# Kernel tuning notes

Measured on AMD Instinct MI355X. Metric: run time of the kernel, lower is better.

## Reference

```python
import jax, jax.numpy as jnp
import numpy as np

N_QUBITS = 8
INPUT_DIM = 256
SEQ_LEN = 256
BATCH = 512


def qgate(theta, x):
    # Closed-form expectation of the PennyLane circuit:
    #   RX(x_i) then RY(theta_i) on each wire (from |0>), then CNOT chain 0->1->...->n-1,
    #   measure <Z_k>.  Single-wire <Z_j> = cos(x_j) * cos(theta_j); CNOT chain maps
    #   Z_k -> Z_0 Z_1 ... Z_k in the Heisenberg picture, so on the product state
    #   <Z_k> = prod_{j<=k} cos(x_j) cos(theta_j).
    # x: (B, n_wires), theta: (n_wires,)
    return jnp.cumprod(jnp.cos(x) * jnp.cos(theta), axis=-1)


def setup_inputs() -> dict:
    key = jax.random.key(0)
    ks = jax.random.split(key, 14)
    d_in = INPUT_DIM + N_QUBITS  # concat([x, hx]) -> 264
    lin_scale = 1.0 / np.sqrt(d_in)
    inp = {
        "inputs": jax.random.normal(ks[0], (SEQ_LEN, BATCH, INPUT_DIM), dtype=jnp.float32),
        "Wf": jax.random.normal(ks[1], (N_QUBITS, d_in), dtype=jnp.float32) * lin_scale,
        "bf": jax.random.normal(ks[2], (N_QUBITS,), dtype=jnp.float32) * lin_scale,
        "Wi": jax.random.normal(ks[3], (N_QUBITS, d_in), dtype=jnp.float32) * lin_scale,
        "bi": jax.random.normal(ks[4], (N_QUBITS,), dtype=jnp.float32) * lin_scale,
        "Wu": jax.random.normal(ks[5], (N_QUBITS, d_in), dtype=jnp.float32) * lin_scale,
        "bu": jax.random.normal(ks[6], (N_QUBITS,), dtype=jnp.float32) * lin_scale,
        "Wo": jax.random.normal(ks[7], (N_QUBITS, d_in), dtype=jnp.float32) * lin_scale,
        "bo": jax.random.normal(ks[8], (N_QUBITS,), dtype=jnp.float32) * lin_scale,
        "pf": jax.random.normal(ks[9], (N_QUBITS,), dtype=jnp.float32),
        "pi_": jax.random.normal(ks[10], (N_QUBITS,), dtype=jnp.float32),
        "pu": jax.random.normal(ks[11], (N_QUBITS,), dtype=jnp.float32),
        "po": jax.random.normal(ks[12], (N_QUBITS,), dtype=jnp.float32),
    }
    return inp


def reference(inputs, Wf, bf, Wi, bi, Wu, bu, Wo, bo, pf, pi_, pu, po):
    B = inputs.shape[1]
    H = pf.shape[0]  # hidden_dim == n_qubits

    def step(carry, x):
        hx, cx = carry
        comb = jnp.concatenate([x, hx], axis=1)  # (B, input_dim + H)
        f = jax.nn.sigmoid(qgate(pf, comb @ Wf.T + bf))
        i = jax.nn.sigmoid(qgate(pi_, comb @ Wi.T + bi))
        g = jnp.tanh(qgate(pu, comb @ Wu.T + bu))
        o = jax.nn.sigmoid(qgate(po, comb @ Wo.T + bo))
        cx = f * cx + i * g
        hx = o * jnp.tanh(cx)
        return (hx, cx), hx

    init = (jnp.zeros((B, H), dtype=inputs.dtype), jnp.zeros((B, H), dtype=inputs.dtype))
    (hx, cx), stacked = jax.lax.scan(step, init, inputs)
    return stacked, hx, cx
```

## Files before the change

kernel.cpp:

```cpp
#include <hip/hip_runtime.h>
#include <hip/hip_bf16.h>


#define SEQ   256
#define BATCH 512
#define DIN   256
#define NROWS (SEQ * BATCH)
#define DCOMB 264
#define ZSTR  34

typedef __attribute__((ext_vector_type(8))) short short8;
typedef __attribute__((ext_vector_type(4))) float f32x4;
typedef __attribute__((ext_vector_type(2))) float f32x2;

__device__ __forceinline__ short f2bf(float f) {
    union { __hip_bfloat16 h; short s; } u;
    u.h = __float2bfloat16(f);
    return u.s;
}
__device__ __forceinline__ float bf2f(short s) {
    union { short s; __hip_bfloat16 h; } u;
    u.s = s;
    return __bfloat162float(u.h);
}

__device__ __forceinline__ short8 pack8(float4 a, float4 b) {
    union { short8 s8; int i[4]; } u;
    union { __hip_bfloat162 h; int i; } v;
    v.h = __float22bfloat162_rn(make_float2(a.x, a.y)); u.i[0] = v.i;
    v.h = __float22bfloat162_rn(make_float2(a.z, a.w)); u.i[1] = v.i;
    v.h = __float22bfloat162_rn(make_float2(b.x, b.y)); u.i[2] = v.i;
    v.h = __float22bfloat162_rn(make_float2(b.z, b.w)); u.i[3] = v.i;
    return u.s8;
}

#define DPP_ROR(V, S) \
    __int_as_float(__builtin_amdgcn_update_dpp(__float_as_int(V), __float_as_int(V), 0x120 | (S), 0xF, 0xF, false))
#define QP(V, CTRL) \
    __int_as_float(__builtin_amdgcn_update_dpp(__float_as_int(V), __float_as_int(V), (CTRL), 0xF, 0xF, false))
#define PSTG2(A, D) { \
    float s0_ = __int_as_float(__builtin_amdgcn_update_dpp(one_i, __float_as_int(A.x), 0x110 | (D), 0xF, 0xF, false)); \
    float s1_ = __int_as_float(__builtin_amdgcn_update_dpp(one_i, __float_as_int(A.y), 0x110 | (D), 0xF, 0xF, false)); \
    A *= (f32x2){s0_, s1_}; }

__global__ __launch_bounds__(512, 2) void qlstm_fused(
    const float* __restrict__ X,
    const float* __restrict__ Wf, const float* __restrict__ Wi,
    const float* __restrict__ Wu, const float* __restrict__ Wo,
    const float* __restrict__ bfv, const float* __restrict__ biv,
    const float* __restrict__ buv, const float* __restrict__ bov,
    const float* __restrict__ pf, const float* __restrict__ pi_,
    const float* __restrict__ pu, const float* __restrict__ po,
    float* __restrict__ out)
{
    __shared__ short8 Wl[2048];
    __shared__ float Zl[516 * ZSTR];
    __shared__ float Hl[SEQ * 16];

    const int tx  = threadIdx.x;
    const int l   = tx & 63;
    const int wid = tx >> 6;
    const int lm  = l & 15;
    const int lk  = l >> 4;
    const int B0  = blockIdx.x;

    const float* Wg[4] = {Wf, Wi, Wu, Wo};
    const float* Bg[4] = {bfv, biv, buv, bov};

    #pragma unroll
    for (int e = 0; e < 4; ++e) {
        const int ent  = tx + e * 512;
        const int lane = ent & 63;
        const int ks   = (ent >> 6) & 7;
        const int hl   = (ent >> 9) & 1;
        const int nt   = (ent >> 10) & 1;
        const int elm  = lane & 15, elk = lane >> 4;
        const int c    = nt * 16 + elm;
        const float* wrow = Wg[c & 3] + (c >> 2) * DCOMB + ks * 32 + elk * 8;
        short8 fr;
        #pragma unroll
        for (int j = 0; j < 8; ++j) {
            const float v = wrow[j];
            const short h16 = f2bf(v);
            fr[j] = hl ? f2bf(v - bf2f(h16)) : h16;
        }
        Wl[ent] = fr;
    }

    float bias0, bias1;
    { const int c0 = lm;      bias0 = Bg[c0 & 3][c0 >> 2];
      const int c1 = 16 + lm; bias1 = Bg[c1 & 3][c1 >> 2]; }

    __syncthreads();

    #pragma unroll
    for (int p = 0; p < 4; ++p) {
        const int r0 = p * 128 + wid * 16;
        const int r  = r0 + lm;
        const float* xbase =
            X + ((long)(r >> 1) * BATCH + B0 * 2 + (r & 1)) * DIN + lk * 8;

        float4 xv[16];
        #pragma unroll
        for (int i = 0; i < 16; ++i)
            xv[i] = *(const float4*)(xbase + (i >> 1) * 32 + (i & 1) * 4);

        f32x4 acc0 = (f32x4){bias0, bias0, bias0, bias0};
        f32x4 acc1 = (f32x4){bias1, bias1, bias1, bias1};
        #pragma unroll
        for (int ks = 0; ks < 8; ++ks) {
            const short8 a = pack8(xv[2 * ks], xv[2 * ks + 1]);
            acc0 = __builtin_amdgcn_mfma_f32_16x16x32_bf16(a, Wl[ks * 64 + l],        acc0, 0, 0, 0);
            acc0 = __builtin_amdgcn_mfma_f32_16x16x32_bf16(a, Wl[(8  + ks) * 64 + l], acc0, 0, 0, 0);
            acc1 = __builtin_amdgcn_mfma_f32_16x16x32_bf16(a, Wl[(16 + ks) * 64 + l], acc1, 0, 0, 0);
            acc1 = __builtin_amdgcn_mfma_f32_16x16x32_bf16(a, Wl[(24 + ks) * 64 + l], acc1, 0, 0, 0);
        }

        #pragma unroll
        for (int rr = 0; rr < 4; ++rr) {
            Zl[(r0 + lk * 4 + rr) * ZSTR + lm]      = acc0[rr];
            Zl[(r0 + lk * 4 + rr) * ZSTR + 16 + lm] = acc1[rr];
        }
    }
    __syncthreads();

    if (tx < 64) {
        const int q   = tx & 15;
        const int kq  = q >> 1;
        const int hi  = q & 1;
        const int bl  = (tx >> 4) & 1;
        const int b   = B0 * 2 + bl;
        const int oidx = b * 8 + kq;
        const int woff = kq * DCOMB + DIN;

        const float* WgA = hi ? Wu : Wf;
        const float* WgB = hi ? Wo : Wi;
        f32x2 wp[8];
        #pragma unroll
        for (int s = 0; s < 8; ++s) {
            const int j = (kq - s) & 7;
            wp[s] = (f32x2){WgA[woff + j], WgB[woff + j]};
        }
        const f32x2 cth = (f32x2){__cosf((hi ? pu : pf)[kq]),
                                  __cosf((hi ? po : pi_)[kq])};

        const float SK1 = 0.25f, SK2 = -0.0208333333f, SK3 = 0.0020833333f,
                    SK4 = -0.00021082f;
        const f32x2 k0 = (f32x2){hi ? 0.0f : 0.5f, 0.5f};
        const f32x2 k1 = (f32x2){hi ? 0.9999016f : SK1, SK1};
        const f32x2 k2 = (f32x2){hi ? -0.3310485f : SK2, SK2};
        const f32x2 k3 = (f32x2){hi ? 0.1204423f : SK3, SK3};
        const f32x2 k4 = (f32x2){hi ? -0.0277012f : SK4, SK4};

        const int one_i = __float_as_int(1.0f);

        float hx = 0.0f, cx = 0.0f;
        const int zbase = bl * ZSTR + 2 * q;
        float* __restrict__ hlp = Hl + bl * 8 + kq;

        f32x2 ring0 = *(const f32x2*)&Zl[zbase];
        f32x2 ring1 = *(const f32x2*)&Zl[2 * ZSTR + zbase];

        #pragma unroll 8
        for (int t = 0; t < SEQ; ++t) {
            const f32x2 z2 = ring0;
            ring0 = ring1;
            ring1 = *(const f32x2*)&Zl[(t + 2) * (2 * ZSTR) + zbase];

            const float h0 = hx;
            const float h1 = DPP_ROR(hx, 2),  h2 = DPP_ROR(hx, 4);
            const float h3 = DPP_ROR(hx, 6),  h4 = DPP_ROR(hx, 8);
            const float h5 = DPP_ROR(hx, 10), h6 = DPP_ROR(hx, 12);
            const float h7 = DPP_ROR(hx, 14);

            f32x2 e0 = (f32x2){h0, h0} * wp[0] + (f32x2){h1, h1} * wp[1];
            f32x2 e1 = (f32x2){h2, h2} * wp[2] + (f32x2){h3, h3} * wp[3];
            f32x2 e2 = (f32x2){h4, h4} * wp[4] + (f32x2){h5, h5} * wp[5];
            f32x2 e3 = (f32x2){h6, h6} * wp[6] + (f32x2){h7, h7} * wp[7];
            const f32x2 p = ((z2 + e0) + (e1 + e2)) + e3;

            f32x2 A = (f32x2){__cosf(p.x), __cosf(p.y)} * cth;
            PSTG2(A, 2) PSTG2(A, 4) PSTG2(A, 8)

            const f32x2 t2 = A * A;
            f32x2 rr = k3 + t2 * k4;
            rr = k2 + t2 * rr;
            rr = k1 + t2 * rr;
            const f32x2 P = k0 + A * rr;

            const float f_all = QP(P.x, 0xA0);
            const float u_all = QP(P.x, 0xF5);
            const float i_all = QP(P.y, 0xA0);
            const float o_all = QP(P.y, 0xF5);

            cx = fmaf(f_all, cx, i_all * u_all);

            const float tq  = cx * cx;
            const float num = cx * fmaf(tq, fmaf(tq, 1.0f, 105.0f), 945.0f);
            const float den = fmaf(tq, fmaf(tq, 15.0f, 420.0f), 945.0f);
            const float tc  = num * __builtin_amdgcn_rcpf(den);

            hx = o_all * tc;

            hlp[t * 16] = hx;
        }
        if (hi == 0 && tx < 32) {
            out[NROWS * 8 + oidx]        = hx;
            out[NROWS * 8 + 4096 + oidx] = cx;
        }
    }
    __syncthreads();

    {
        const int f0 = tx * 8;
        const int t  = f0 >> 4;
        const int c  = f0 & 15;
        const float4* src = (const float4*)&Hl[f0];
        float4* dst = (float4*)(out + (long)t * (BATCH * 8) + B0 * 16 + c);
        dst[0] = src[0];
        dst[1] = src[1];
    }
}

extern "C" void kernel_launch(void* const* d_in, const int* in_sizes, int n_in,
                              void* d_out, int out_size, void* d_ws, size_t ws_size,
                              hipStream_t stream) {
    const float* X   = (const float*)d_in[0];
    const float* Wf  = (const float*)d_in[1];
    const float* bfv = (const float*)d_in[2];
    const float* Wi  = (const float*)d_in[3];
    const float* biv = (const float*)d_in[4];
    const float* Wu  = (const float*)d_in[5];
    const float* buv = (const float*)d_in[6];
    const float* Wo  = (const float*)d_in[7];
    const float* bov = (const float*)d_in[8];
    const float* pf  = (const float*)d_in[9];
    const float* pi_ = (const float*)d_in[10];
    const float* pu  = (const float*)d_in[11];
    const float* po  = (const float*)d_in[12];
    float* out = (float*)d_out;
    (void)d_ws; (void)ws_size;

    qlstm_fused<<<BATCH / 2, 512, 0, stream>>>(
        X, Wf, Wi, Wu, Wo, bfv, biv, buv, bov, pf, pi_, pu, po, out);
}
```

Measured before the change: 252.0 us.

## Transpose Z and H shared buffers to time-major rows for batched recurrence loads

Lays out the precomputed gate pre-activations in shared memory per lane row with time contiguous, so the serial recurrence loop can fetch eight timesteps with four 16-byte LDS loads, double-buffered one block ahead. Hidden states are collected per eight steps in registers and written as two vector stores by the writer lanes instead of one scalar store per step. The output copy then reads the transposed H buffer with strided scalar LDS reads. The aim is to take per-step LDS latency and store traffic off the latency-bound sequential chain, at the cost of more registers and a heavier epilogue.

```diff
diff --git a/kernel.cpp b/kernel.cpp
--- a/kernel.cpp
+++ b/kernel.cpp
@@ -7,7 +7,8 @@
 #define DIN   256
 #define NROWS (SEQ * BATCH)
 #define DCOMB 264
-#define ZSTR  34
+#define ZTSTR 514
+#define HLSTR 260
 
 typedef __attribute__((ext_vector_type(8))) short short8;
 typedef __attribute__((ext_vector_type(4))) float f32x4;
@@ -42,6 +43,67 @@
     float s0_ = __int_as_float(__builtin_amdgcn_update_dpp(one_i, __float_as_int(A.x), 0x110 | (D), 0xF, 0xF, false)); \
     float s1_ = __int_as_float(__builtin_amdgcn_update_dpp(one_i, __float_as_int(A.y), 0x110 | (D), 0xF, 0xF, false)); \
     A *= (f32x2){s0_, s1_}; }
+
+__device__ __forceinline__ void scan_body8(
+    int T0, const float* __restrict__ zrow, float* __restrict__ hlrow,
+    bool writer, f32x4 (&ZC)[4], f32x4 (&ZN)[4],
+    float& hx, float& cx,
+    const f32x2 (&wp)[8], const f32x2 cth,
+    const f32x2 k0, const f32x2 k1, const f32x2 k2, const f32x2 k3,
+    const f32x2 k4, const int one_i)
+{
+    #pragma unroll
+    for (int j = 0; j < 4; ++j)
+        ZN[j] = *(const f32x4*)&zrow[(T0 + 8) * 2 + j * 4];
+
+    float hxh[8];
+    #pragma unroll
+    for (int u = 0; u < 8; ++u) {
+        const f32x2 z2 = (f32x2){ ZC[u >> 1][(u & 1) * 2],
+                                  ZC[u >> 1][(u & 1) * 2 + 1] };
+
+        const float h0 = hx;
+        const float h1 = DPP_ROR(hx, 2),  h2 = DPP_ROR(hx, 4);
+        const float h3 = DPP_ROR(hx, 6),  h4 = DPP_ROR(hx, 8);
+        const float h5 = DPP_ROR(hx, 10), h6 = DPP_ROR(hx, 12);
+        const float h7 = DPP_ROR(hx, 14);
+
+        f32x2 e0 = (f32x2){h0, h0} * wp[0] + (f32x2){h1, h1} * wp[1];
+        f32x2 e1 = (f32x2){h2, h2} * wp[2] + (f32x2){h3, h3} * wp[3];
+        f32x2 e2 = (f32x2){h4, h4} * wp[4] + (f32x2){h5, h5} * wp[5];
+        f32x2 e3 = (f32x2){h6, h6} * wp[6] + (f32x2){h7, h7} * wp[7];
+        const f32x2 p = ((z2 + e0) + (e1 + e2)) + e3;
+
+        f32x2 A = (f32x2){__cosf(p.x), __cosf(p.y)} * cth;
+        PSTG2(A, 2) PSTG2(A, 4) PSTG2(A, 8)
+
+        const f32x2 t2 = A * A;
+        f32x2 rr = k3 + t2 * k4;
+        rr = k2 + t2 * rr;
+        rr = k1 + t2 * rr;
+        const f32x2 P = k0 + A * rr;
+
+        const float f_all = QP(P.x, 0xA0);
+        const float u_all = QP(P.x, 0xF5);
+        const float i_all = QP(P.y, 0xA0);
+        const float o_all = QP(P.y, 0xF5);
+
+        cx = fmaf(f_all, cx, i_all * u_all);
+
+        const float tq  = cx * cx;
+        const float num = cx * fmaf(tq, fmaf(tq, 1.0f, 105.0f), 945.0f);
+        const float den = fmaf(tq, fmaf(tq, 15.0f, 420.0f), 945.0f);
+        const float tc  = num * __builtin_amdgcn_rcpf(den);
+
+        hx = o_all * tc;
+        hxh[u] = hx;
+    }
+
+    if (writer) {
+        *(f32x4*)&hlrow[T0]     = (f32x4){hxh[0], hxh[1], hxh[2], hxh[3]};
+        *(f32x4*)&hlrow[T0 + 4] = (f32x4){hxh[4], hxh[5], hxh[6], hxh[7]};
+    }
+}
 
 __global__ __launch_bounds__(512, 2) void qlstm_fused(
     const float* __restrict__ X,
@@ -54,8 +116,8 @@
     float* __restrict__ out)
 {
     __shared__ short8 Wl[2048];
-    __shared__ float Zl[516 * ZSTR];
-    __shared__ float Hl[SEQ * 16];
+    __shared__ float Zt[32 * ZTSTR + 16];
+    __shared__ float Hl2[16 * HLSTR];
 
     const int tx  = threadIdx.x;
     const int l   = tx & 63;
@@ -118,8 +180,10 @@
 
         #pragma unroll
         for (int rr = 0; rr < 4; ++rr) {
-            Zl[(r0 + lk * 4 + rr) * ZSTR + lm]      = acc0[rr];
-            Zl[(r0 + lk * 4 + rr) * ZSTR + 16 + lm] = acc1[rr];
+            const int rw = r0 + lk * 4 + rr;
+            const int tt = rw >> 1, blw = rw & 1;
+            Zt[(blw * 16 + (lm >> 1)) * ZTSTR + tt * 2 + (lm & 1)]     = acc0[rr];
+            Zt[(blw * 16 + 8 + (lm >> 1)) * ZTSTR + tt * 2 + (lm & 1)] = acc1[rr];
         }
     }
     __syncthreads();
@@ -155,55 +219,21 @@
         const int one_i = __float_as_int(1.0f);
 
         float hx = 0.0f, cx = 0.0f;
-        const int zbase = bl * ZSTR + 2 * q;
-        float* __restrict__ hlp = Hl + bl * 8 + kq;
-
-        f32x2 ring0 = *(const f32x2*)&Zl[zbase];
-        f32x2 ring1 = *(const f32x2*)&Zl[2 * ZSTR + zbase];
-
-        #pragma unroll 8
-        for (int t = 0; t < SEQ; ++t) {
-            const f32x2 z2 = ring0;
-            ring0 = ring1;
-            ring1 = *(const f32x2*)&Zl[(t + 2) * (2 * ZSTR) + zbase];
-
-            const float h0 = hx;
-            const float h1 = DPP_ROR(hx, 2),  h2 = DPP_ROR(hx, 4);
-            const float h3 = DPP_ROR(hx, 6),  h4 = DPP_ROR(hx, 8);
-            const float h5 = DPP_ROR(hx, 10), h6 = DPP_ROR(hx, 12);
-            const float h7 = DPP_ROR(hx, 14);
-
-            f32x2 e0 = (f32x2){h0, h0} * wp[0] + (f32x2){h1, h1} * wp[1];
-            f32x2 e1 = (f32x2){h2, h2} * wp[2] + (f32x2){h3, h3} * wp[3];
-            f32x2 e2 = (f32x2){h4, h4} * wp[4] + (f32x2){h5, h5} * wp[5];
-            f32x2 e3 = (f32x2){h6, h6} * wp[6] + (f32x2){h7, h7} * wp[7];
-            const f32x2 p = ((z2 + e0) + (e1 + e2)) + e3;
-
-            f32x2 A = (f32x2){__cosf(p.x), __cosf(p.y)} * cth;
-            PSTG2(A, 2) PSTG2(A, 4) PSTG2(A, 8)
-
-            const f32x2 t2 = A * A;
-            f32x2 rr = k3 + t2 * k4;
-            rr = k2 + t2 * rr;
-            rr = k1 + t2 * rr;
-            const f32x2 P = k0 + A * rr;
-
-            const float f_all = QP(P.x, 0xA0);
-            const float u_all = QP(P.x, 0xF5);
-            const float i_all = QP(P.y, 0xA0);
-            const float o_all = QP(P.y, 0xF5);
-
-            cx = fmaf(f_all, cx, i_all * u_all);
-
-            const float tq  = cx * cx;
-            const float num = cx * fmaf(tq, fmaf(tq, 1.0f, 105.0f), 945.0f);
-            const float den = fmaf(tq, fmaf(tq, 15.0f, 420.0f), 945.0f);
-            const float tc  = num * __builtin_amdgcn_rcpf(den);
-
-            hx = o_all * tc;
-
-            hlp[t * 16] = hx;
-        }
+        const float* __restrict__ zrow = &Zt[(bl * 16 + q) * ZTSTR];
+        float* __restrict__ hlrow = &Hl2[(bl * 8 + kq) * HLSTR];
+        const bool writer = (hi == 0) && (tx < 32);
+
+        f32x4 zbA[4], zbB[4];
+        #pragma unroll
+        for (int j = 0; j < 4; ++j) zbA[j] = *(const f32x4*)&zrow[j * 4];
+
+        for (int t0 = 0; t0 < SEQ; t0 += 16) {
+            scan_body8(t0,     zrow, hlrow, writer, zbA, zbB, hx, cx,
+                       wp, cth, k0, k1, k2, k3, k4, one_i);
+            scan_body8(t0 + 8, zrow, hlrow, writer, zbB, zbA, hx, cx,
+                       wp, cth, k0, k1, k2, k3, k4, one_i);
+        }
+
         if (hi == 0 && tx < 32) {
             out[NROWS * 8 + oidx]        = hx;
             out[NROWS * 8 + 4096 + oidx] = cx;
@@ -214,11 +244,19 @@
     {
         const int f0 = tx * 8;
         const int t  = f0 >> 4;
-        const int c  = f0 & 15;
-        const float4* src = (const float4*)&Hl[f0];
-        float4* dst = (float4*)(out + (long)t * (BATCH * 8) + B0 * 16 + c);
-        dst[0] = src[0];
-        dst[1] = src[1];
+        const int c0 = f0 & 15;
+        float4 v0, v1;
+        v0.x = Hl2[(c0 + 0) * HLSTR + t];
+        v0.y = Hl2[(c0 + 1) * HLSTR + t];
+        v0.z = Hl2[(c0 + 2) * HLSTR + t];
+        v0.w = Hl2[(c0 + 3) * HLSTR + t];
+        v1.x = Hl2[(c0 + 4) * HLSTR + t];
+        v1.y = Hl2[(c0 + 5) * HLSTR + t];
+        v1.z = Hl2[(c0 + 6) * HLSTR + t];
+        v1.w = Hl2[(c0 + 7) * HLSTR + t];
+        float4* dst = (float4*)(out + (long)t * (BATCH * 8) + B0 * 16 + c0);
+        dst[0] = v0;
+        dst[1] = v1;
     }
 }
 
```

New measurement: 249.9 us. No clear change (-0.8%).
